# Performance work log

Measured on AMD Instinct MI355X. Metric: run time of the kernel, lower is better.

The kernel has to match this reference:

```python
import jax, jax.numpy as jnp
import numpy as np

B, H, E, L = 2048, 4096, 8, 512
TAU = 1.0


def setup_inputs() -> dict:
    key = jax.random.key(0)
    k1, k2, k3, k4 = jax.random.split(key, 4)
    hidden = jax.random.normal(k1, (B, H), dtype=jnp.float32)
    envs = jax.random.normal(k2, (B, E), dtype=jnp.float32)
    idx = jnp.arange(B, dtype=jnp.int64)
    gumbel = jax.random.gumbel(k3, (B, E), dtype=jnp.float32)
    W = jax.random.normal(k4, (E, L, H), dtype=jnp.float32) * (1.0 / np.sqrt(H))
    return {"hidden": hidden, "envs": envs, "idx": idx, "gumbel": gumbel, "W": W}


def _hard_gumbel_softmax(log_probs, gumbel, tau):
    # F.gumbel_softmax(log_probs, tau=1, hard=True) with pre-sampled gumbel noise
    y_soft = jax.nn.softmax((log_probs + gumbel) / tau, axis=-1)
    y_hard = jax.nn.one_hot(jnp.argmax(y_soft, axis=-1), y_soft.shape[-1], dtype=y_soft.dtype)
    # straight-through estimator
    return y_hard + y_soft - jax.lax.stop_gradient(y_soft)


def reference(hidden, envs, idx, gumbel, W):
    # gating: env = gumbel_softmax(log_softmax(envs[idx]))  -> [B, E]
    log_probs = jax.nn.log_softmax(envs[idx], axis=-1)
    env = _hard_gumbel_softmax(log_probs, gumbel, TAU)
    # per-expert logits: [B, E, L]; fuses the per-sample python loop
    expert_logits = jnp.einsum("bh,elh->bel", hidden, W)
    # gating combine: [B, L]
    logits = jnp.einsum("be,bel->bl", env, expert_logits)
    # variance penalty over expert weights
    W_mean = jnp.mean(W, axis=0)  # [L, H]
    diff_sq = jnp.sum((W - W_mean[None]) ** 2, axis=(1, 2))  # ||W_e - W_mean||_2^2 per expert
    l1 = jnp.sum(jnp.abs(W), axis=(1, 2))                    # ||W_e||_1 per expert
    loss_penalty = jnp.mean(diff_sq / (l1 ** 2))
    return logits, loss_penalty
```

## Files before the change

kernel.cpp:

```cpp
#include <hip/hip_runtime.h>
#include <hip/hip_bf16.h>

constexpr int B = 2048, H = 4096, E = 8, L = 512;

typedef float f4v __attribute__((ext_vector_type(4)));
typedef short short8 __attribute__((ext_vector_type(8)));

constexpr int BT = 128;
constexpr int LT = 128;
constexpr int KT = 32;
constexpr int SK = 4;
constexpr int RTMAX = 3;
constexpr int NITER = (H / SK) / KT;

constexpr int NGEMM = 8 * 4 * 4 * 3;
constexpr int NPEN = 2048;

constexpr size_t WS_COUNTS = 0;
constexpr size_t WS_ACCUM = 32;
constexpr size_t WS_ROWLIST = 96;
constexpr size_t WS_ZERO_BYTES = 96;

using as1_u32 = const __attribute__((address_space(1))) unsigned int;
using as3_u32 = __attribute__((address_space(3))) unsigned int;

static __device__ __forceinline__ void dma16(const float* g, float* lds) {
  __builtin_amdgcn_global_load_lds((as1_u32*)g, (as3_u32*)lds, 16, 0, 0);
}

static __device__ __forceinline__ unsigned pk2(float a, float b) {
  __hip_bfloat162 p = __float22bfloat162_rn(make_float2(a, b));
  unsigned u;
  __builtin_memcpy(&u, &p, 4);
  return u;
}

static __device__ __forceinline__ short8 cvt8(f4v lo, f4v hi) {
  union { short8 s; unsigned u[4]; } r;
  r.u[0] = pk2(lo.x, lo.y);
  r.u[1] = pk2(lo.z, lo.w);
  r.u[2] = pk2(hi.x, hi.y);
  r.u[3] = pk2(hi.z, hi.w);
  return r.s;
}

__global__ void gating_kernel(const float* __restrict__ envs,
                              const float* __restrict__ gumbel,
                              int* __restrict__ counts,
                              int* __restrict__ row_list) {
  int b = blockIdx.x * blockDim.x + threadIdx.x;
  if (b >= B) return;
  float zmax = -1e30f;
  int am = 0;
#pragma unroll
  for (int e = 0; e < E; ++e) {
    float z = envs[b * E + e] + gumbel[b * E + e];
    if (z > zmax) { zmax = z; am = e; }
  }
  int pos = atomicAdd(&counts[am], 1);
  row_list[am * B + pos] = b;
}

__launch_bounds__(256, 3)
__global__ void fused_kernel(const float* __restrict__ hidden,
                             const float* __restrict__ W,
                             const int* __restrict__ counts,
                             const int* __restrict__ row_list,
                             float* __restrict__ out,
                             float* __restrict__ accum) {
  const int id = blockIdx.x;
  const int t = threadIdx.x;

  __shared__ __align__(16) float AshF[BT * KT];
  __shared__ __align__(16) float BshF[LT * KT];
  __shared__ int rlsh[BT];
  __shared__ float red[4][16];

  if (id >= NGEMM) {
    constexpr int LH = L * H;
    const int p = (id - NGEMM) * 256 + t;

    float4 w[E];
    float mx = 0.f, my = 0.f, mz = 0.f, mw = 0.f;
#pragma unroll
    for (int e = 0; e < E; ++e) {
      w[e] = *(const float4*)(W + (size_t)e * LH + (size_t)p * 4);
      mx += w[e].x; my += w[e].y; mz += w[e].z; mw += w[e].w;
    }
    mx *= 0.125f; my *= 0.125f; mz *= 0.125f; mw *= 0.125f;

    float vals[16];
#pragma unroll
    for (int e = 0; e < E; ++e) {
      float dx = w[e].x - mx, dy = w[e].y - my, dz = w[e].z - mz,
            dw = w[e].w - mw;
      vals[e] = dx * dx + dy * dy + dz * dz + dw * dw;
      vals[8 + e] =
          fabsf(w[e].x) + fabsf(w[e].y) + fabsf(w[e].z) + fabsf(w[e].w);
    }
#pragma unroll
    for (int k = 0; k < 16; ++k) {
      float v = vals[k];
      for (int off = 32; off > 0; off >>= 1) v += __shfl_xor(v, off);
      vals[k] = v;
    }
    const int wave = t >> 6, lane = t & 63;
    if (lane == 0) {
#pragma unroll
      for (int k = 0; k < 16; ++k) red[wave][k] = vals[k];
    }
    __syncthreads();
    if (t < 16) {
      atomicAdd(&accum[t], red[0][t] + red[1][t] + red[2][t] + red[3][t]);
    }
    return;
  }

  const int lt = id & 3;
  const int ep = (id >> 2) & 1;
  const int sk = (id >> 3) & 3;
  const int eh = (id >> 5) & 3;
  const int rt = id >> 7;
  const int e = eh * 2 + ep;

  const int cnt = counts[e];
  const int rbase = rt * BT;
  if (rbase >= cnt) return;
  const int lbase = lt * LT;

  if (t < BT) {
    int rr = rbase + t;
    rlsh[t] = row_list[e * B + (rr < cnt ? rr : (cnt - 1))];
  }
  __syncthreads();

  const float* Wp = W + (size_t)e * L * H + (size_t)lbase * H;

  const int wave = t >> 6;
  const int lane = t & 63;
  const int quad = lane >> 4;
  const int l16 = lane & 15;
  const int wm = (wave >> 1) * 64;
  const int wn = (wave & 1) * 64;

  const int kbeg = sk * (H / SK);
  const int srow = lane >> 3;
  const int sblk = lane & 7;

  const float* sp[8];
  float* sl[8];
  const bool stageA = (wave < 2);
#pragma unroll
  for (int i = 0; i < 8; ++i) {
    int r = (stageA ? wave : (wave - 2)) * 64 + i * 8 + srow;
    int gblk = sblk ^ (r & 7);
    if (stageA) {
      sp[i] = hidden + (size_t)rlsh[r] * H + kbeg + gblk * 4;
      sl[i] = &AshF[(r - srow) * KT];
    } else {
      sp[i] = Wp + (size_t)r * H + kbeg + gblk * 4;
      sl[i] = &BshF[(r - srow) * KT];
    }
  }

  const int r7 = l16 & 7;
  const int slo = (2 * quad) ^ r7;
  const int shi = slo ^ 1;

  f4v acc[4][4] = {};

  for (int it = 0; it < NITER; ++it) {
#pragma unroll
    for (int i = 0; i < 8; ++i) {
      dma16(sp[i], sl[i]);
      sp[i] += KT;
    }
    __syncthreads();

    short8 af[4], bf[4];
#pragma unroll
    for (int i = 0; i < 4; ++i) {
      int ra = wm + i * 16 + l16;
      f4v lo = *(const f4v*)&AshF[ra * KT + slo * 4];
      f4v hi = *(const f4v*)&AshF[ra * KT + shi * 4];
      af[i] = cvt8(lo, hi);
    }
#pragma unroll
    for (int j = 0; j < 4; ++j) {
      int rb = wn + j * 16 + l16;
      f4v lo = *(const f4v*)&BshF[rb * KT + slo * 4];
      f4v hi = *(const f4v*)&BshF[rb * KT + shi * 4];
      bf[j] = cvt8(lo, hi);
    }
#pragma unroll
    for (int i = 0; i < 4; ++i)
#pragma unroll
      for (int j = 0; j < 4; ++j)
        acc[i][j] =
            __builtin_amdgcn_mfma_f32_16x16x32_bf16(af[i], bf[j], acc[i][j],
                                                    0, 0, 0);
    __syncthreads();
  }

#pragma unroll
  for (int i = 0; i < 4; ++i) {
#pragma unroll
    for (int j = 0; j < 4; ++j) {
#pragma unroll
      for (int reg = 0; reg < 4; ++reg) {
        int rloc = wm + i * 16 + quad * 4 + reg;
        if (rbase + rloc < cnt) {
          int bidx = rlsh[rloc];
          atomicAdd(&out[(size_t)bidx * L + lbase + wn + j * 16 + l16],
                    acc[i][j][reg]);
        }
      }
    }
  }
}

__global__ void finalize_kernel(const float* __restrict__ accum,
                                float* __restrict__ out) {
  if (threadIdx.x == 0) {
    float loss = 0.f;
#pragma unroll
    for (int e = 0; e < E; ++e) {
      float l1 = accum[8 + e];
      loss += accum[e] / (l1 * l1);
    }
    out[(size_t)B * L] = loss * 0.125f;
  }
}

extern "C" void kernel_launch(void* const* d_in, const int* in_sizes, int n_in,
                              void* d_out, int out_size, void* d_ws, size_t ws_size,
                              hipStream_t stream) {
  (void)in_sizes; (void)n_in; (void)ws_size;
  const float* hidden = (const float*)d_in[0];
  const float* envs   = (const float*)d_in[1];
  const float* gumbel = (const float*)d_in[3];
  const float* W      = (const float*)d_in[4];
  float* out = (float*)d_out;

  char* ws = (char*)d_ws;
  int*   counts   = (int*)(ws + WS_COUNTS);
  float* accum    = (float*)(ws + WS_ACCUM);
  int*   row_list = (int*)(ws + WS_ROWLIST);

  (void)hipMemsetAsync(d_ws, 0, WS_ZERO_BYTES, stream);
  (void)hipMemsetAsync(d_out, 0, (size_t)out_size * sizeof(float), stream);

  gating_kernel<<<dim3(B / 256), dim3(256), 0, stream>>>(envs, gumbel, counts,
                                                         row_list);

  fused_kernel<<<dim3(NGEMM + NPEN), dim3(256), 0, stream>>>(
      hidden, W, counts, row_list, out, accum);

  finalize_kernel<<<dim3(1), dim3(64), 0, stream>>>(accum, out);
}
```

Measured before the change: 187.2 us.

## Replace LDS-staged GEMM tiles with per-wave direct register loads and double buffering

The shared-memory staging (global_load_lds DMA plus two barriers per K step) is removed from the gated expert GEMM. Each wave now owns an independent 64x64 output tile and loads bf16-converted fragments straight from global memory into registers, double-buffered across two K chunks. The grid is remapped (8 L tiles of 64, two 256-row groups per expert) and occupancy hint lowered to 2 blocks/CU. This eliminates barrier and LDS costs, but each wave re-fetches W rows that other waves in its block also read, so cache reuse replaces explicit LDS sharing and register pressure increases.

After: 209.5 us. 12.0% more time.

```diff
diff --git a/kernel.cpp b/kernel.cpp
--- a/kernel.cpp
+++ b/kernel.cpp
@@ -2,31 +2,21 @@
 #include <hip/hip_bf16.h>
 
 constexpr int B = 2048, H = 4096, E = 8, L = 512;
+constexpr int LH = L * H;
 
 typedef float f4v __attribute__((ext_vector_type(4)));
 typedef short short8 __attribute__((ext_vector_type(8)));
 
-constexpr int BT = 128;
-constexpr int LT = 128;
+constexpr int SK = 4;
+constexpr int KSPAN = H / SK;
 constexpr int KT = 32;
-constexpr int SK = 4;
-constexpr int RTMAX = 3;
-constexpr int NITER = (H / SK) / KT;
-
-constexpr int NGEMM = 8 * 4 * 4 * 3;
+constexpr int NGEMM = 8 * 8 * 4 * 2;
 constexpr int NPEN = 2048;
 
 constexpr size_t WS_COUNTS = 0;
 constexpr size_t WS_ACCUM = 32;
 constexpr size_t WS_ROWLIST = 96;
 constexpr size_t WS_ZERO_BYTES = 96;
-
-using as1_u32 = const __attribute__((address_space(1))) unsigned int;
-using as3_u32 = __attribute__((address_space(3))) unsigned int;
-
-static __device__ __forceinline__ void dma16(const float* g, float* lds) {
-  __builtin_amdgcn_global_load_lds((as1_u32*)g, (as3_u32*)lds, 16, 0, 0);
-}
 
 static __device__ __forceinline__ unsigned pk2(float a, float b) {
   __hip_bfloat162 p = __float22bfloat162_rn(make_float2(a, b));
@@ -35,7 +25,7 @@
   return u;
 }
 
-static __device__ __forceinline__ short8 cvt8(f4v lo, f4v hi) {
+static __device__ __forceinline__ short8 cvt8(float4 lo, float4 hi) {
   union { short8 s; unsigned u[4]; } r;
   r.u[0] = pk2(lo.x, lo.y);
   r.u[1] = pk2(lo.z, lo.w);
@@ -61,7 +51,7 @@
   row_list[am * B + pos] = b;
 }
 
-__launch_bounds__(256, 3)
+__launch_bounds__(256, 2)
 __global__ void fused_kernel(const float* __restrict__ hidden,
                              const float* __restrict__ W,
                              const int* __restrict__ counts,
@@ -71,13 +61,8 @@
   const int id = blockIdx.x;
   const int t = threadIdx.x;
 
-  __shared__ __align__(16) float AshF[BT * KT];
-  __shared__ __align__(16) float BshF[LT * KT];
-  __shared__ int rlsh[BT];
-  __shared__ float red[4][16];
-
   if (id >= NGEMM) {
-    constexpr int LH = L * H;
+    __shared__ float red[4][16];
     const int p = (id - NGEMM) * 256 + t;
 
     float4 w[E];
@@ -104,10 +89,10 @@
       for (int off = 32; off > 0; off >>= 1) v += __shfl_xor(v, off);
       vals[k] = v;
     }
-    const int wave = t >> 6, lane = t & 63;
+    const int wv = t >> 6, lane = t & 63;
     if (lane == 0) {
 #pragma unroll
-      for (int k = 0; k < 16; ++k) red[wave][k] = vals[k];
+      for (int k = 0; k < 16; ++k) red[wv][k] = vals[k];
     }
     __syncthreads();
     if (t < 16) {
@@ -116,82 +101,58 @@
     return;
   }
 
-  const int lt = id & 3;
-  const int ep = (id >> 2) & 1;
-  const int sk = (id >> 3) & 3;
-  const int eh = (id >> 5) & 3;
-  const int rt = id >> 7;
-  const int e = eh * 2 + ep;
+  const int e   = id & 7;
+  const int lt  = (id >> 3) & 7;
+  const int sk  = (id >> 6) & 3;
+  const int rtb = (id >> 8) & 1;
 
   const int cnt = counts[e];
-  const int rbase = rt * BT;
-  if (rbase >= cnt) return;
-  const int lbase = lt * LT;
-
-  if (t < BT) {
-    int rr = rbase + t;
-    rlsh[t] = row_list[e * B + (rr < cnt ? rr : (cnt - 1))];
-  }
-  __syncthreads();
-
-  const float* Wp = W + (size_t)e * L * H + (size_t)lbase * H;
-
   const int wave = t >> 6;
   const int lane = t & 63;
   const int quad = lane >> 4;
   const int l16 = lane & 15;
-  const int wm = (wave >> 1) * 64;
-  const int wn = (wave & 1) * 64;
-
-  const int kbeg = sk * (H / SK);
-  const int srow = lane >> 3;
-  const int sblk = lane & 7;
-
-  const float* sp[8];
-  float* sl[8];
-  const bool stageA = (wave < 2);
-#pragma unroll
-  for (int i = 0; i < 8; ++i) {
-    int r = (stageA ? wave : (wave - 2)) * 64 + i * 8 + srow;
-    int gblk = sblk ^ (r & 7);
-    if (stageA) {
-      sp[i] = hidden + (size_t)rlsh[r] * H + kbeg + gblk * 4;
-      sl[i] = &AshF[(r - srow) * KT];
-    } else {
-      sp[i] = Wp + (size_t)r * H + kbeg + gblk * 4;
-      sl[i] = &BshF[(r - srow) * KT];
-    }
-  }
-
-  const int r7 = l16 & 7;
-  const int slo = (2 * quad) ^ r7;
-  const int shi = slo ^ 1;
+
+  const int rbase = rtb * 256 + wave * 64;
+  if (rbase >= cnt) return;
+  const int lbase = lt * 64;
+
+  const int kbeg = sk * KSPAN;
+  const int koff0 = kbeg + quad * 8;
+
+  const float* ap[4];
+  const float* bp[4];
+#pragma unroll
+  for (int i = 0; i < 4; ++i) {
+    int gr = rbase + i * 16 + l16;
+    gr = gr < cnt ? gr : (cnt - 1);
+    int bidx = row_list[e * B + gr];
+    ap[i] = hidden + (size_t)bidx * H + koff0;
+    bp[i] = W + (size_t)e * LH + (size_t)(lbase + i * 16 + l16) * H + koff0;
+  }
 
   f4v acc[4][4] = {};
 
-  for (int it = 0; it < NITER; ++it) {
-#pragma unroll
-    for (int i = 0; i < 8; ++i) {
-      dma16(sp[i], sl[i]);
-      sp[i] += KT;
-    }
-    __syncthreads();
-
+  float4 aL0[4], aH0[4], bL0[4], bH0[4];
+  float4 aL1[4], aH1[4], bL1[4], bH1[4];
+
+  auto load_chunk = [&](float4* aL, float4* aH, float4* bL, float4* bH,
+                        int k) {
+#pragma unroll
+    for (int p = 0; p < 4; ++p) {
+      aL[p] = *(const float4*)(ap[p] + k);
+      aH[p] = *(const float4*)(ap[p] + k + 4);
+      bL[p] = *(const float4*)(bp[p] + k);
+      bH[p] = *(const float4*)(bp[p] + k + 4);
+    }
+  };
+
+  auto compute = [&](const float4* aL, const float4* aH, const float4* bL,
+                     const float4* bH) {
     short8 af[4], bf[4];
 #pragma unroll
-    for (int i = 0; i < 4; ++i) {
-      int ra = wm + i * 16 + l16;
-      f4v lo = *(const f4v*)&AshF[ra * KT + slo * 4];
-      f4v hi = *(const f4v*)&AshF[ra * KT + shi * 4];
-      af[i] = cvt8(lo, hi);
-    }
-#pragma unroll
-    for (int j = 0; j < 4; ++j) {
-      int rb = wn + j * 16 + l16;
-      f4v lo = *(const f4v*)&BshF[rb * KT + slo * 4];
-      f4v hi = *(const f4v*)&BshF[rb * KT + shi * 4];
-      bf[j] = cvt8(lo, hi);
-    }
+    for (int i = 0; i < 4; ++i) af[i] = cvt8(aL[i], aH[i]);
+#pragma unroll
+    for (int j = 0; j < 4; ++j) bf[j] = cvt8(bL[j], bH[j]);
 #pragma unroll
     for (int i = 0; i < 4; ++i)
 #pragma unroll
@@ -199,19 +160,35 @@
         acc[i][j] =
             __builtin_amdgcn_mfma_f32_16x16x32_bf16(af[i], bf[j], acc[i][j],
                                                     0, 0, 0);
-    __syncthreads();
-  }
-
+  };
+
+  load_chunk(aL0, aH0, bL0, bH0, 0);
+  load_chunk(aL1, aH1, bL1, bH1, KT);
+
+  for (int k = 0; k < KSPAN; k += 2 * KT) {
+    compute(aL0, aH0, bL0, bH0);
+    if (k + 2 * KT < KSPAN) load_chunk(aL0, aH0, bL0, bH0, k + 2 * KT);
+    compute(aL1, aH1, bL1, bH1);
+    if (k + 3 * KT < KSPAN) load_chunk(aL1, aH1, bL1, bH1, k + 3 * KT);
+  }
+
+  int bout[4][4];
+#pragma unroll
+  for (int i = 0; i < 4; ++i)
+#pragma unroll
+    for (int reg = 0; reg < 4; ++reg) {
+      int grow = rbase + i * 16 + quad * 4 + reg;
+      bout[i][reg] = (grow < cnt) ? row_list[e * B + grow] : -1;
+    }
 #pragma unroll
   for (int i = 0; i < 4; ++i) {
 #pragma unroll
     for (int j = 0; j < 4; ++j) {
 #pragma unroll
       for (int reg = 0; reg < 4; ++reg) {
-        int rloc = wm + i * 16 + quad * 4 + reg;
-        if (rbase + rloc < cnt) {
-          int bidx = rlsh[rloc];
-          atomicAdd(&out[(size_t)bidx * L + lbase + wn + j * 16 + l16],
+        int bidx = bout[i][reg];
+        if (bidx >= 0) {
+          atomicAdd(&out[(size_t)bidx * L + lbase + j * 16 + l16],
                     acc[i][j][reg]);
         }
       }
```

## Double-buffer LDS tiles in the expert GEMM to overlap loads with MFMA

Applied to the files above, without the earlier changes.

Splits the A and B shared-memory tiles into two buffers so the next K-slice is fetched by global_load_lds while the current slice is converted to bf16 and fed to MFMA. This also removes the trailing barrier, leaving one barrier per iteration. The aim is to hide global-load latency behind compute. In exchange, LDS per block doubles, so launch bounds drop from 3 to 2 blocks per CU, which lowers occupancy and the latency hiding that came from running more blocks.

After: 180.8 us. 1.04x faster.

```diff
diff --git a/kernel.cpp b/kernel.cpp
--- a/kernel.cpp
+++ b/kernel.cpp
@@ -2,6 +2,7 @@
 #include <hip/hip_bf16.h>
 
 constexpr int B = 2048, H = 4096, E = 8, L = 512;
+constexpr int LH = L * H;
 
 typedef float f4v __attribute__((ext_vector_type(4)));
 typedef short short8 __attribute__((ext_vector_type(8)));
@@ -13,7 +14,7 @@
 constexpr int RTMAX = 3;
 constexpr int NITER = (H / SK) / KT;
 
-constexpr int NGEMM = 8 * 4 * 4 * 3;
+constexpr int NGEMM = 4 * 2 * 4 * 4 * RTMAX;
 constexpr int NPEN = 2048;
 
 constexpr size_t WS_COUNTS = 0;
@@ -61,7 +62,7 @@
   row_list[am * B + pos] = b;
 }
 
-__launch_bounds__(256, 3)
+__launch_bounds__(256, 2)
 __global__ void fused_kernel(const float* __restrict__ hidden,
                              const float* __restrict__ W,
                              const int* __restrict__ counts,
@@ -71,13 +72,12 @@
   const int id = blockIdx.x;
   const int t = threadIdx.x;
 
-  __shared__ __align__(16) float AshF[BT * KT];
-  __shared__ __align__(16) float BshF[LT * KT];
+  __shared__ __align__(16) float AshF[2][BT * KT];
+  __shared__ __align__(16) float BshF[2][LT * KT];
   __shared__ int rlsh[BT];
   __shared__ float red[4][16];
 
   if (id >= NGEMM) {
-    constexpr int LH = L * H;
     const int p = (id - NGEMM) * 256 + t;
 
     float4 w[E];
@@ -104,10 +104,10 @@
       for (int off = 32; off > 0; off >>= 1) v += __shfl_xor(v, off);
       vals[k] = v;
     }
-    const int wave = t >> 6, lane = t & 63;
+    const int wv = t >> 6, lane = t & 63;
     if (lane == 0) {
 #pragma unroll
-      for (int k = 0; k < 16; ++k) red[wave][k] = vals[k];
+      for (int k = 0; k < 16; ++k) red[wv][k] = vals[k];
     }
     __syncthreads();
     if (t < 16) {
@@ -134,7 +134,7 @@
   }
   __syncthreads();
 
-  const float* Wp = W + (size_t)e * L * H + (size_t)lbase * H;
+  const float* Wp = W + (size_t)e * LH + (size_t)lbase * H;
 
   const int wave = t >> 6;
   const int lane = t & 63;
@@ -148,7 +148,7 @@
   const int sblk = lane & 7;
 
   const float* sp[8];
-  float* sl[8];
+  float* sl[2][8];
   const bool stageA = (wave < 2);
 #pragma unroll
   for (int i = 0; i < 8; ++i) {
@@ -156,12 +156,22 @@
     int gblk = sblk ^ (r & 7);
     if (stageA) {
       sp[i] = hidden + (size_t)rlsh[r] * H + kbeg + gblk * 4;
-      sl[i] = &AshF[(r - srow) * KT];
+      sl[0][i] = &AshF[0][(r - srow) * KT];
+      sl[1][i] = &AshF[1][(r - srow) * KT];
     } else {
       sp[i] = Wp + (size_t)r * H + kbeg + gblk * 4;
-      sl[i] = &BshF[(r - srow) * KT];
-    }
-  }
+      sl[0][i] = &BshF[0][(r - srow) * KT];
+      sl[1][i] = &BshF[1][(r - srow) * KT];
+    }
+  }
+
+  auto stage = [&](int buf) {
+#pragma unroll
+    for (int i = 0; i < 8; ++i) {
+      dma16(sp[i], sl[buf][i]);
+      sp[i] += KT;
+    }
+  };
 
   const int r7 = l16 & 7;
   const int slo = (2 * quad) ^ r7;
@@ -169,27 +179,26 @@
 
   f4v acc[4][4] = {};
 
+  stage(0);
+
   for (int it = 0; it < NITER; ++it) {
-#pragma unroll
-    for (int i = 0; i < 8; ++i) {
-      dma16(sp[i], sl[i]);
-      sp[i] += KT;
-    }
+    const int buf = it & 1;
     __syncthreads();
+    if (it + 1 < NITER) stage(buf ^ 1);
 
     short8 af[4], bf[4];
 #pragma unroll
     for (int i = 0; i < 4; ++i) {
       int ra = wm + i * 16 + l16;
-      f4v lo = *(const f4v*)&AshF[ra * KT + slo * 4];
-      f4v hi = *(const f4v*)&AshF[ra * KT + shi * 4];
+      f4v lo = *(const f4v*)&AshF[buf][ra * KT + slo * 4];
+      f4v hi = *(const f4v*)&AshF[buf][ra * KT + shi * 4];
       af[i] = cvt8(lo, hi);
     }
 #pragma unroll
     for (int j = 0; j < 4; ++j) {
       int rb = wn + j * 16 + l16;
-      f4v lo = *(const f4v*)&BshF[rb * KT + slo * 4];
-      f4v hi = *(const f4v*)&BshF[rb * KT + shi * 4];
+      f4v lo = *(const f4v*)&BshF[buf][rb * KT + slo * 4];
+      f4v hi = *(const f4v*)&BshF[buf][rb * KT + shi * 4];
       bf[j] = cvt8(lo, hi);
     }
 #pragma unroll
@@ -199,7 +208,6 @@
         acc[i][j] =
             __builtin_amdgcn_mfma_f32_16x16x32_bf16(af[i], bf[j], acc[i][j],
                                                     0, 0, 0);
-    __syncthreads();
   }
 
 #pragma unroll
```
